# Optimization experiments

Hardware: AMD Instinct MI355X
Metric: run time of the kernel (lower is better)

## Reference

```python
import jax, jax.numpy as jnp
import numpy as np

DK = 64  # embedding_size / h = 1024 / 16


def setup_inputs() -> dict:
    key = jax.random.key(0)
    k1, k2, k3 = jax.random.split(key, 3)
    S = 8192
    return {
        "q": jax.random.normal(k1, (S, DK), dtype=jnp.float32),
        "k": jax.random.normal(k2, (S, DK), dtype=jnp.float32),
        "v": jax.random.normal(k3, (S, DK), dtype=jnp.float32),
    }


def reference(q, k, v):
    # scores: [S, S]; NOTE: source scales by 1/dk (not 1/sqrt(dk)) — kept faithful.
    qk = jnp.matmul(q, k.T) * (1.0 / DK)
    S = qk.shape[0]
    # causal mask: position (i, j) allowed iff i >= j (0 added), else -inf
    i = jnp.arange(S)[:, None]
    j = jnp.arange(S)[None, :]
    qk = jnp.where(i >= j, qk, -jnp.inf)
    attn = jax.nn.softmax(qk, axis=-1)
    return jnp.matmul(attn, v)
```

## Files before the change

### kernel.cpp

```cpp
#include <hip/hip_runtime.h>
#include <hip/hip_bf16.h>

#define S_LEN 8192
#define DKD   64
#define BM    64
#define BN    64
#define PAD   8
#define LDK   (DKD + PAD)

#define CHUNK 512
#define NC    (S_LEN / CHUNK)
#define NWORK 1088

#define WS_NEED ((size_t)2 * S_LEN * DKD * 2 + (size_t)NC * S_LEN * 4 + (size_t)NC * S_LEN * DKD * 2)

typedef __bf16 bf16x8 __attribute__((ext_vector_type(8)));
typedef float  f32x4  __attribute__((ext_vector_type(4)));
typedef unsigned short ushort8v __attribute__((ext_vector_type(8)));
typedef unsigned short ushort4v __attribute__((ext_vector_type(4)));

__device__ __forceinline__ unsigned short f2bf(float f) {
  union { float f; unsigned u; } v; v.f = f;
  unsigned u = v.u;
  return (unsigned short)((u + 0x7fffu + ((u >> 16) & 1u)) >> 16);
}
__device__ __forceinline__ float bf2f(unsigned short s) {
  union { unsigned u; float f; } v; v.u = ((unsigned)s) << 16;
  return v.f;
}
__device__ __forceinline__ unsigned pk2(float a, float b) {
  union { float f; unsigned u; } x, y; x.f = a; y.f = b;
  return ((x.u + 0x8000u) >> 16) | ((y.u + 0x8000u) & 0xffff0000u);
}
__device__ __forceinline__ bf16x8 q_frag8(const float* p, float sc) {
  float4 u = *(const float4*)p;
  float4 w = *(const float4*)(p + 4);
  union { ushort8v s; bf16x8 b; } r;
  r.s[0] = f2bf(u.x * sc); r.s[1] = f2bf(u.y * sc);
  r.s[2] = f2bf(u.z * sc); r.s[3] = f2bf(u.w * sc);
  r.s[4] = f2bf(w.x * sc); r.s[5] = f2bf(w.y * sc);
  r.s[6] = f2bf(w.z * sc); r.s[7] = f2bf(w.w * sc);
  return r.b;
}

__global__ __launch_bounds__(256) void precompute(const float* __restrict__ k,
                                                  const float* __restrict__ v,
                                                  unsigned short* __restrict__ Kb,
                                                  unsigned short* __restrict__ Vtb) {
  __shared__ unsigned short Ls[64][72];
  const int b = blockIdx.x, tid = threadIdx.x;
  if (blockIdx.y == 0) {
    size_t base = (size_t)b * 64 * DKD;
#pragma unroll
    for (int j = 0; j < 4; ++j) {
      int vi = tid + j * 256;
      float4 x = *(const float4*)(k + base + (size_t)vi * 4);
      ushort4v o = { f2bf(x.x), f2bf(x.y), f2bf(x.z), f2bf(x.w) };
      *(ushort4v*)(Kb + base + (size_t)vi * 4) = o;
    }
  } else {
#pragma unroll
    for (int j = 0; j < 4; ++j) {
      int vi = tid + j * 256;
      int row = vi >> 4, c4 = vi & 15;
      float4 x = *(const float4*)(v + ((size_t)(b * 64 + row)) * DKD + c4 * 4);
      Ls[row][c4 * 4 + 0] = f2bf(x.x);
      Ls[row][c4 * 4 + 1] = f2bf(x.y);
      Ls[row][c4 * 4 + 2] = f2bf(x.z);
      Ls[row][c4 * 4 + 3] = f2bf(x.w);
    }
    __syncthreads();
#pragma unroll
    for (int j = 0; j < 4; ++j) {
      int ci = tid + j * 256;
      int d = ci >> 4, c0 = ci & 15;
      int kl = c0 * 4;
      int s0 = ((((kl & 7) >> 2) + 2 * (kl >> 5)) << 4) + (((kl >> 3) & 3) << 2);
      ushort4v o = { Ls[s0][d], Ls[s0 + 1][d], Ls[s0 + 2][d], Ls[s0 + 3][d] };
      *(ushort4v*)(Vtb + (size_t)d * S_LEN + b * 64 + kl) = o;
    }
  }
}

__global__ __launch_bounds__(256) void attn_partial(const float* __restrict__ qg,
                                                    const unsigned short* __restrict__ Kb,
                                                    const unsigned short* __restrict__ Vtb,
                                                    unsigned short* __restrict__ Opart,
                                                    float* __restrict__ l_ws) {
  const int w = blockIdx.x;
  int g = (int)((sqrtf((float)w + 1.0f) - 1.0f) * 0.5f);
  while (4 * (g + 1) * (g + 2) <= w) ++g;
  while (4 * g * (g + 1) > w) --g;
  const int r0  = w - 4 * g * (g + 1);
  const int qq  = r0 / (g + 1);
  const int qt  = 8 * g + qq;
  const int cch = r0 - qq * (g + 1);

  const int q0 = qt * BM, chunk0 = cch * CHUNK;
  const int n_kt = min(CHUNK / BN, qt - 8 * cch + 1);

  __shared__ __align__(16) unsigned short Ks[BN][LDK];
  __shared__ __align__(16) unsigned short Vts[DKD][LDK];

  const int tid = threadIdx.x, wave = tid >> 6, lane = tid & 63;
  const int col = lane & 15, quad = lane >> 4;

  const int qidx = q0 + wave * 16 + col;
  const float* qp = qg + (size_t)qidx * DKD;
  bf16x8 b0 = q_frag8(qp + quad * 8, 1.0f / 64.0f);
  bf16x8 b1 = q_frag8(qp + 32 + quad * 8, 1.0f / 64.0f);

  const int srow0 = tid >> 3, sch = tid & 7;
  const int srow1 = srow0 + 32;
  const unsigned short* kbase = Kb + (size_t)chunk0 * DKD;
  const unsigned short* vbase = Vtb + chunk0;

  {
    *(ushort8v*)&Ks[srow0][sch * 8]  = *(const ushort8v*)(kbase + (size_t)srow0 * DKD + sch * 8);
    *(ushort8v*)&Ks[srow1][sch * 8]  = *(const ushort8v*)(kbase + (size_t)srow1 * DKD + sch * 8);
    *(ushort8v*)&Vts[srow0][sch * 8] = *(const ushort8v*)(vbase + (size_t)srow0 * S_LEN + sch * 8);
    *(ushort8v*)&Vts[srow1][sch * 8] = *(const ushort8v*)(vbase + (size_t)srow1 * S_LEN + sch * 8);
  }
  __syncthreads();

  float lsum = 0.0f;
  f32x4 Of[4];
#pragma unroll
  for (int i = 0; i < 4; ++i) Of[i] = f32x4{0.0f, 0.0f, 0.0f, 0.0f};

  ushort8v Kp0, Kp1, Vp0, Vp1;
  for (int it = 0; it < n_kt; ++it) {
    const int k0 = chunk0 + it * BN;
    const bool pf = (it + 1 < n_kt);

    if (pf) {
      const size_t noff = (size_t)(it + 1) * BN;
      Kp0 = *(const ushort8v*)(kbase + (noff + srow0) * DKD + sch * 8);
      Kp1 = *(const ushort8v*)(kbase + (noff + srow1) * DKD + sch * 8);
      Vp0 = *(const ushort8v*)(vbase + (size_t)srow0 * S_LEN + noff + sch * 8);
      Vp1 = *(const ushort8v*)(vbase + (size_t)srow1 * S_LEN + noff + sch * 8);
    }

    f32x4 Sf[4];
#pragma unroll
    for (int t = 0; t < 4; ++t) {
      const unsigned short* kr = &Ks[t * 16 + col][quad * 8];
      f32x4 acc = f32x4{0.0f, 0.0f, 0.0f, 0.0f};
      acc = __builtin_amdgcn_mfma_f32_16x16x32_bf16(*(const bf16x8*)kr, b0, acc, 0, 0, 0);
      acc = __builtin_amdgcn_mfma_f32_16x16x32_bf16(*(const bf16x8*)(kr + 32), b1, acc, 0, 0, 0);
      Sf[t] = acc;
    }

#pragma unroll
    for (int t = 0; t < 4; ++t) {
      int kb = k0 + t * 16 + quad * 4;
#pragma unroll
      for (int r = 0; r < 4; ++r) {
        float p = __expf(Sf[t][r]);
        p = (kb + r <= qidx) ? p : 0.0f;
        Sf[t][r] = p;
        lsum += p;
      }
    }

    union { unsigned u[4]; bf16x8 b; } pa0, pa1;
    pa0.u[0] = pk2(Sf[0][0], Sf[0][1]); pa0.u[1] = pk2(Sf[0][2], Sf[0][3]);
    pa0.u[2] = pk2(Sf[1][0], Sf[1][1]); pa0.u[3] = pk2(Sf[1][2], Sf[1][3]);
    pa1.u[0] = pk2(Sf[2][0], Sf[2][1]); pa1.u[1] = pk2(Sf[2][2], Sf[2][3]);
    pa1.u[2] = pk2(Sf[3][0], Sf[3][1]); pa1.u[3] = pk2(Sf[3][2], Sf[3][3]);

#pragma unroll
    for (int dt = 0; dt < 4; ++dt) {
      const unsigned short* vr = &Vts[dt * 16 + col][quad * 8];
      Of[dt] = __builtin_amdgcn_mfma_f32_16x16x32_bf16(pa0.b, *(const bf16x8*)vr, Of[dt], 0, 0, 0);
      Of[dt] = __builtin_amdgcn_mfma_f32_16x16x32_bf16(pa1.b, *(const bf16x8*)(vr + 32), Of[dt], 0, 0, 0);
    }

    if (pf) {
      __syncthreads();
      *(ushort8v*)&Ks[srow0][sch * 8]  = Kp0;
      *(ushort8v*)&Ks[srow1][sch * 8]  = Kp1;
      *(ushort8v*)&Vts[srow0][sch * 8] = Vp0;
      *(ushort8v*)&Vts[srow1][sch * 8] = Vp1;
      __syncthreads();
    }
  }

  lsum += __shfl_xor(lsum, 16);
  lsum += __shfl_xor(lsum, 32);
  if (lane < 16)
    l_ws[cch * S_LEN + q0 + wave * 16 + lane] = lsum;

#pragma unroll
  for (int r = 0; r < 4; ++r) {
    int rowg = q0 + wave * 16 + quad * 4 + r;
    uint2 o2;
    o2.x = pk2(Of[0][r], Of[1][r]);
    o2.y = pk2(Of[2][r], Of[3][r]);
    *(uint2*)(Opart + ((size_t)cch * S_LEN + rowg) * DKD + col * 4) = o2;
  }
}

__global__ __launch_bounds__(256) void attn_merge(const unsigned short* __restrict__ Opart,
                                                  const float* __restrict__ l_ws,
                                                  float* __restrict__ out) {
  int idx = blockIdx.x * 256 + threadIdx.x;
  int row = idx >> 3, m = idx & 7;
  int nc = (row >> 9) + 1;

  float acc[8] = {0, 0, 0, 0, 0, 0, 0, 0};
  float L = 0.0f;
  for (int c = 0; c < nc; ++c) {
    L += l_ws[c * S_LEN + row];
    ushort8v o = *(const ushort8v*)(Opart + ((size_t)c * S_LEN + row) * DKD + m * 8);
#pragma unroll
    for (int j = 0; j < 8; ++j) acc[j] += bf2f(o[j]);
  }
  float inv = 1.0f / L;
#pragma unroll
  for (int j0 = 0; j0 < 4; ++j0) {
    float2 w2 = { acc[j0] * inv, acc[j0 + 4] * inv };
    *(float2*)(out + (size_t)row * DKD + 16 * j0 + 2 * m) = w2;
  }
}

__global__ __launch_bounds__(128) void attn_fwd(const float* __restrict__ qg,
                                                const float* __restrict__ kg,
                                                const float* __restrict__ vg,
                                                float* __restrict__ out) {
  __shared__ __align__(16) unsigned short Qs[32][LDK];
  __shared__ __align__(16) unsigned short Ksh[BN][LDK];
  __shared__ __align__(16) unsigned short Vt[DKD][LDK];
  __shared__ __align__(16) unsigned short Ps[2][16][LDK];

  const int tid = threadIdx.x, wave = tid >> 6, lane = tid & 63;
  const int col = lane & 15, quad = lane >> 4;
  const int q0 = blockIdx.x * 32;

#pragma unroll
  for (int r = 0; r < 4; ++r) {
    int vi = tid + r * 128;
    int row = vi >> 4, c4 = vi & 15;
    if (row < 32) {
      float4 val = *(const float4*)(qg + (size_t)(q0 + row) * DKD + c4 * 4);
      Qs[row][c4 * 4 + 0] = f2bf(val.x);
      Qs[row][c4 * 4 + 1] = f2bf(val.y);
      Qs[row][c4 * 4 + 2] = f2bf(val.z);
      Qs[row][c4 * 4 + 3] = f2bf(val.w);
    }
  }

  float m_run[4], l_run[4];
  f32x4 Of[4];
#pragma unroll
  for (int i = 0; i < 4; ++i) {
    m_run[i] = -1e30f; l_run[i] = 0.0f;
    Of[i] = f32x4{0.0f, 0.0f, 0.0f, 0.0f};
  }

  const int n_tiles = (q0 + 31) / BN + 1;
  for (int it = 0; it < n_tiles; ++it) {
    __syncthreads();
    const int k0 = it * BN;
#pragma unroll
    for (int r = 0; r < 8; ++r) {
      int vi = tid + r * 128;
      int row = vi >> 4, c4 = vi & 15;
      float4 kv = *(const float4*)(kg + (size_t)(k0 + row) * DKD + c4 * 4);
      Ksh[row][c4 * 4 + 0] = f2bf(kv.x);
      Ksh[row][c4 * 4 + 1] = f2bf(kv.y);
      Ksh[row][c4 * 4 + 2] = f2bf(kv.z);
      Ksh[row][c4 * 4 + 3] = f2bf(kv.w);
      float4 vv = *(const float4*)(vg + (size_t)(k0 + row) * DKD + c4 * 4);
      Vt[c4 * 4 + 0][row] = f2bf(vv.x);
      Vt[c4 * 4 + 1][row] = f2bf(vv.y);
      Vt[c4 * 4 + 2][row] = f2bf(vv.z);
      Vt[c4 * 4 + 3][row] = f2bf(vv.w);
    }
    __syncthreads();

    f32x4 Sf[4];
    const unsigned short* qrow = &Qs[wave * 16 + col][0];
#pragma unroll
    for (int t = 0; t < 4; ++t) {
      f32x4 acc = f32x4{0.0f, 0.0f, 0.0f, 0.0f};
#pragma unroll
      for (int c = 0; c < 2; ++c) {
        bf16x8 a = *(const bf16x8*)(qrow + c * 32 + quad * 8);
        bf16x8 b = *(const bf16x8*)(&Ksh[t * 16 + col][c * 32 + quad * 8]);
        acc = __builtin_amdgcn_mfma_f32_16x16x32_bf16(a, b, acc, 0, 0, 0);
      }
      Sf[t] = acc;
    }

    const float scale = 1.0f / 64.0f;
    float rmax[4] = {-1e30f, -1e30f, -1e30f, -1e30f};
#pragma unroll
    for (int t = 0; t < 4; ++t) {
      int kidx = k0 + t * 16 + col;
#pragma unroll
      for (int r = 0; r < 4; ++r) {
        int qidx = q0 + wave * 16 + quad * 4 + r;
        float s = Sf[t][r] * scale;
        s = (kidx <= qidx) ? s : -1e30f;
        Sf[t][r] = s;
        rmax[r] = fmaxf(rmax[r], s);
      }
    }
#pragma unroll
    for (int off = 1; off <= 8; off <<= 1)
#pragma unroll
      for (int r = 0; r < 4; ++r)
        rmax[r] = fmaxf(rmax[r], __shfl_xor(rmax[r], off));

    float alpha[4], rsum[4];
#pragma unroll
    for (int r = 0; r < 4; ++r) {
      float mn = fmaxf(m_run[r], rmax[r]);
      alpha[r] = __expf(m_run[r] - mn);
      m_run[r] = mn;
      rsum[r] = 0.0f;
    }
#pragma unroll
    for (int t = 0; t < 4; ++t)
#pragma unroll
      for (int r = 0; r < 4; ++r) {
        float p = __expf(Sf[t][r] - m_run[r]);
        Sf[t][r] = p;
        rsum[r] += p;
      }
#pragma unroll
    for (int off = 1; off <= 8; off <<= 1)
#pragma unroll
      for (int r = 0; r < 4; ++r)
        rsum[r] += __shfl_xor(rsum[r], off);
#pragma unroll
    for (int r = 0; r < 4; ++r)
      l_run[r] = l_run[r] * alpha[r] + rsum[r];
#pragma unroll
    for (int dt = 0; dt < 4; ++dt)
#pragma unroll
      for (int r = 0; r < 4; ++r)
        Of[dt][r] *= alpha[r];

#pragma unroll
    for (int t = 0; t < 4; ++t)
#pragma unroll
      for (int r = 0; r < 4; ++r)
        Ps[wave][quad * 4 + r][t * 16 + col] = f2bf(Sf[t][r]);
    __syncthreads();

    const unsigned short* prow = &Ps[wave][col][0];
#pragma unroll
    for (int dt = 0; dt < 4; ++dt) {
#pragma unroll
      for (int c = 0; c < 2; ++c) {
        bf16x8 a = *(const bf16x8*)(prow + c * 32 + quad * 8);
        bf16x8 b = *(const bf16x8*)(&Vt[dt * 16 + col][c * 32 + quad * 8]);
        Of[dt] = __builtin_amdgcn_mfma_f32_16x16x32_bf16(a, b, Of[dt], 0, 0, 0);
      }
    }
  }

#pragma unroll
  for (int r = 0; r < 4; ++r) {
    float inv = 1.0f / l_run[r];
    int qrow_g = q0 + wave * 16 + quad * 4 + r;
#pragma unroll
    for (int dt = 0; dt < 4; ++dt)
      out[(size_t)qrow_g * DKD + dt * 16 + col] = Of[dt][r] * inv;
  }
}

extern "C" void kernel_launch(void* const* d_in, const int* in_sizes, int n_in,
                              void* d_out, int out_size, void* d_ws, size_t ws_size,
                              hipStream_t stream) {
  const float* q = (const float*)d_in[0];
  const float* k = (const float*)d_in[1];
  const float* v = (const float*)d_in[2];
  float* out = (float*)d_out;

  if (ws_size >= WS_NEED) {
    unsigned short* Kb  = (unsigned short*)d_ws;
    unsigned short* Vtb = Kb + (size_t)S_LEN * DKD;
    float* l_ws         = (float*)(Vtb + (size_t)S_LEN * DKD);
    unsigned short* Opart = (unsigned short*)(l_ws + (size_t)NC * S_LEN);

    hipLaunchKernelGGL(precompute, dim3(S_LEN / 64, 2), dim3(256), 0, stream, k, v, Kb, Vtb);
    hipLaunchKernelGGL(attn_partial, dim3(NWORK), dim3(256), 0, stream,
                       q, Kb, Vtb, Opart, l_ws);
    hipLaunchKernelGGL(attn_merge, dim3(S_LEN * 8 / 256), dim3(256), 0, stream,
                       Opart, l_ws, out);
  } else {
    hipLaunchKernelGGL(attn_fwd, dim3(S_LEN / 32), dim3(128), 0, stream, q, k, v, out);
  }
}
```

Measured before the change: 90.05 us.

## Widen key tile to 128 and schedule heaviest work items first

Doubles the key/value tile per inner iteration from 64 to 128. The V-transpose precompute is reworked so each block handles a 128-key by 32-dim slab with a matching permuted layout. This halves the number of barrier-separated iterations and raises MFMA work per synchronisation, at the cost of more registers and LDS per block. Work items are also issued in reverse order so the longest causal rows start first, which should reduce tail imbalance. Causal masking now operates at 128-key granularity, so slightly more fully-masked keys are computed.

After: 90.57 us. No clear change (+0.6%).

```diff
diff --git a/kernel.cpp b/kernel.cpp
--- a/kernel.cpp
+++ b/kernel.cpp
@@ -4,7 +4,7 @@
 #define S_LEN 8192
 #define DKD   64
 #define BM    64
-#define BN    64
+#define BN    128
 #define PAD   8
 #define LDK   (DKD + PAD)
 
@@ -47,7 +47,7 @@
                                                   const float* __restrict__ v,
                                                   unsigned short* __restrict__ Kb,
                                                   unsigned short* __restrict__ Vtb) {
-  __shared__ unsigned short Ls[64][72];
+  __shared__ unsigned short Ls[128][36];
   const int b = blockIdx.x, tid = threadIdx.x;
   if (blockIdx.y == 0) {
     size_t base = (size_t)b * 64 * DKD;
@@ -59,11 +59,12 @@
       *(ushort4v*)(Kb + base + (size_t)vi * 4) = o;
     }
   } else {
+    const int tile = b >> 1, dh = (b & 1) * 32;
 #pragma unroll
     for (int j = 0; j < 4; ++j) {
       int vi = tid + j * 256;
-      int row = vi >> 4, c4 = vi & 15;
-      float4 x = *(const float4*)(v + ((size_t)(b * 64 + row)) * DKD + c4 * 4);
+      int row = vi >> 3, c4 = vi & 7;
+      float4 x = *(const float4*)(v + ((size_t)(tile * 128 + row)) * DKD + dh + c4 * 4);
       Ls[row][c4 * 4 + 0] = f2bf(x.x);
       Ls[row][c4 * 4 + 1] = f2bf(x.y);
       Ls[row][c4 * 4 + 2] = f2bf(x.z);
@@ -73,11 +74,10 @@
 #pragma unroll
     for (int j = 0; j < 4; ++j) {
       int ci = tid + j * 256;
-      int d = ci >> 4, c0 = ci & 15;
-      int kl = c0 * 4;
-      int s0 = ((((kl & 7) >> 2) + 2 * (kl >> 5)) << 4) + (((kl >> 3) & 3) << 2);
-      ushort4v o = { Ls[s0][d], Ls[s0 + 1][d], Ls[s0 + 2][d], Ls[s0 + 3][d] };
-      *(ushort4v*)(Vtb + (size_t)d * S_LEN + b * 64 + kl) = o;
+      int dloc = ci >> 5, kq = ci & 31;
+      int s0 = 32 * (kq >> 3) + 16 * (kq & 1) + 4 * ((kq >> 1) & 3);
+      ushort4v o = { Ls[s0][dloc], Ls[s0 + 1][dloc], Ls[s0 + 2][dloc], Ls[s0 + 3][dloc] };
+      *(ushort4v*)(Vtb + (size_t)(dh + dloc) * S_LEN + tile * 128 + kq * 4) = o;
     }
   }
 }
@@ -87,20 +87,20 @@
                                                     const unsigned short* __restrict__ Vtb,
                                                     unsigned short* __restrict__ Opart,
                                                     float* __restrict__ l_ws) {
-  const int w = blockIdx.x;
-  int g = (int)((sqrtf((float)w + 1.0f) - 1.0f) * 0.5f);
-  while (4 * (g + 1) * (g + 2) <= w) ++g;
-  while (4 * g * (g + 1) > w) --g;
-  const int r0  = w - 4 * g * (g + 1);
+  const int wr = (NWORK - 1) - blockIdx.x;
+  int g = (int)((sqrtf((float)wr + 1.0f) - 1.0f) * 0.5f);
+  while (4 * (g + 1) * (g + 2) <= wr) ++g;
+  while (4 * g * (g + 1) > wr) --g;
+  const int r0  = wr - 4 * g * (g + 1);
   const int qq  = r0 / (g + 1);
   const int qt  = 8 * g + qq;
   const int cch = r0 - qq * (g + 1);
 
   const int q0 = qt * BM, chunk0 = cch * CHUNK;
-  const int n_kt = min(CHUNK / BN, qt - 8 * cch + 1);
-
-  __shared__ __align__(16) unsigned short Ks[BN][LDK];
-  __shared__ __align__(16) unsigned short Vts[DKD][LDK];
+  const int n_kt = min(CHUNK / BN, ((q0 - chunk0) >> 7) + 1);
+
+  __shared__ __align__(16) unsigned short Ks[BN][72];
+  __shared__ __align__(16) unsigned short Vts[DKD][136];
 
   const int tid = threadIdx.x, wave = tid >> 6, lane = tid & 63;
   const int col = lane & 15, quad = lane >> 4;
@@ -110,16 +110,17 @@
   bf16x8 b0 = q_frag8(qp + quad * 8, 1.0f / 64.0f);
   bf16x8 b1 = q_frag8(qp + 32 + quad * 8, 1.0f / 64.0f);
 
-  const int srow0 = tid >> 3, sch = tid & 7;
-  const int srow1 = srow0 + 32;
+  const int krow = tid >> 3, kch = tid & 7;
+  const int vd   = tid >> 4, vch = tid & 15;
   const unsigned short* kbase = Kb + (size_t)chunk0 * DKD;
   const unsigned short* vbase = Vtb + chunk0;
 
-  {
-    *(ushort8v*)&Ks[srow0][sch * 8]  = *(const ushort8v*)(kbase + (size_t)srow0 * DKD + sch * 8);
-    *(ushort8v*)&Ks[srow1][sch * 8]  = *(const ushort8v*)(kbase + (size_t)srow1 * DKD + sch * 8);
-    *(ushort8v*)&Vts[srow0][sch * 8] = *(const ushort8v*)(vbase + (size_t)srow0 * S_LEN + sch * 8);
-    *(ushort8v*)&Vts[srow1][sch * 8] = *(const ushort8v*)(vbase + (size_t)srow1 * S_LEN + sch * 8);
+#pragma unroll
+  for (int j = 0; j < 4; ++j) {
+    *(ushort8v*)&Ks[krow + j * 32][kch * 8] =
+        *(const ushort8v*)(kbase + (size_t)(krow + j * 32) * DKD + kch * 8);
+    *(ushort8v*)&Vts[vd + j * 16][vch * 8] =
+        *(const ushort8v*)(vbase + (size_t)(vd + j * 16) * S_LEN + vch * 8);
   }
   __syncthreads();
 
@@ -128,22 +129,23 @@
 #pragma unroll
   for (int i = 0; i < 4; ++i) Of[i] = f32x4{0.0f, 0.0f, 0.0f, 0.0f};
 
-  ushort8v Kp0, Kp1, Vp0, Vp1;
+  ushort8v Kp[4], Vp[4];
   for (int it = 0; it < n_kt; ++it) {
     const int k0 = chunk0 + it * BN;
     const bool pf = (it + 1 < n_kt);
 
     if (pf) {
       const size_t noff = (size_t)(it + 1) * BN;
-      Kp0 = *(const ushort8v*)(kbase + (noff + srow0) * DKD + sch * 8);
-      Kp1 = *(const ushort8v*)(kbase + (noff + srow1) * DKD + sch * 8);
-      Vp0 = *(const ushort8v*)(vbase + (size_t)srow0 * S_LEN + noff + sch * 8);
-      Vp1 = *(const ushort8v*)(vbase + (size_t)srow1 * S_LEN + noff + sch * 8);
-    }
-
-    f32x4 Sf[4];
-#pragma unroll
-    for (int t = 0; t < 4; ++t) {
+#pragma unroll
+      for (int j = 0; j < 4; ++j) {
+        Kp[j] = *(const ushort8v*)(kbase + (noff + krow + j * 32) * DKD + kch * 8);
+        Vp[j] = *(const ushort8v*)(vbase + (size_t)(vd + j * 16) * S_LEN + noff + vch * 8);
+      }
+    }
+
+    f32x4 Sf[8];
+#pragma unroll
+    for (int t = 0; t < 8; ++t) {
       const unsigned short* kr = &Ks[t * 16 + col][quad * 8];
       f32x4 acc = f32x4{0.0f, 0.0f, 0.0f, 0.0f};
       acc = __builtin_amdgcn_mfma_f32_16x16x32_bf16(*(const bf16x8*)kr, b0, acc, 0, 0, 0);
@@ -152,7 +154,7 @@
     }
 
 #pragma unroll
-    for (int t = 0; t < 4; ++t) {
+    for (int t = 0; t < 8; ++t) {
       int kb = k0 + t * 16 + quad * 4;
 #pragma unroll
       for (int r = 0; r < 4; ++r) {
@@ -163,25 +165,30 @@
       }
     }
 
-    union { unsigned u[4]; bf16x8 b; } pa0, pa1;
-    pa0.u[0] = pk2(Sf[0][0], Sf[0][1]); pa0.u[1] = pk2(Sf[0][2], Sf[0][3]);
-    pa0.u[2] = pk2(Sf[1][0], Sf[1][1]); pa0.u[3] = pk2(Sf[1][2], Sf[1][3]);
-    pa1.u[0] = pk2(Sf[2][0], Sf[2][1]); pa1.u[1] = pk2(Sf[2][2], Sf[2][3]);
-    pa1.u[2] = pk2(Sf[3][0], Sf[3][1]); pa1.u[3] = pk2(Sf[3][2], Sf[3][3]);
+    union { unsigned u[4]; bf16x8 b; } pa[4];
+#pragma unroll
+    for (int m = 0; m < 4; ++m) {
+      pa[m].u[0] = pk2(Sf[2 * m][0], Sf[2 * m][1]);
+      pa[m].u[1] = pk2(Sf[2 * m][2], Sf[2 * m][3]);
+      pa[m].u[2] = pk2(Sf[2 * m + 1][0], Sf[2 * m + 1][1]);
+      pa[m].u[3] = pk2(Sf[2 * m + 1][2], Sf[2 * m + 1][3]);
+    }
 
 #pragma unroll
     for (int dt = 0; dt < 4; ++dt) {
       const unsigned short* vr = &Vts[dt * 16 + col][quad * 8];
-      Of[dt] = __builtin_amdgcn_mfma_f32_16x16x32_bf16(pa0.b, *(const bf16x8*)vr, Of[dt], 0, 0, 0);
-      Of[dt] = __builtin_amdgcn_mfma_f32_16x16x32_bf16(pa1.b, *(const bf16x8*)(vr + 32), Of[dt], 0, 0, 0);
+#pragma unroll
+      for (int m = 0; m < 4; ++m)
+        Of[dt] = __builtin_amdgcn_mfma_f32_16x16x32_bf16(pa[m].b, *(const bf16x8*)(vr + m * 32), Of[dt], 0, 0, 0);
     }
 
     if (pf) {
       __syncthreads();
-      *(ushort8v*)&Ks[srow0][sch * 8]  = Kp0;
-      *(ushort8v*)&Ks[srow1][sch * 8]  = Kp1;
-      *(ushort8v*)&Vts[srow0][sch * 8] = Vp0;
-      *(ushort8v*)&Vts[srow1][sch * 8] = Vp1;
+#pragma unroll
+      for (int j = 0; j < 4; ++j) {
+        *(ushort8v*)&Ks[krow + j * 32][kch * 8]  = Kp[j];
+        *(ushort8v*)&Vts[vd + j * 16][vch * 8]   = Vp[j];
+      }
       __syncthreads();
     }
   }
@@ -229,7 +236,7 @@
                                                 const float* __restrict__ vg,
                                                 float* __restrict__ out) {
   __shared__ __align__(16) unsigned short Qs[32][LDK];
-  __shared__ __align__(16) unsigned short Ksh[BN][LDK];
+  __shared__ __align__(16) unsigned short Ksh[64][LDK];
   __shared__ __align__(16) unsigned short Vt[DKD][LDK];
   __shared__ __align__(16) unsigned short Ps[2][16][LDK];
 
@@ -258,10 +265,10 @@
     Of[i] = f32x4{0.0f, 0.0f, 0.0f, 0.0f};
   }
 
-  const int n_tiles = (q0 + 31) / BN + 1;
+  const int n_tiles = (q0 + 31) / 64 + 1;
   for (int it = 0; it < n_tiles; ++it) {
     __syncthreads();
-    const int k0 = it * BN;
+    const int k0 = it * 64;
 #pragma unroll
     for (int r = 0; r < 8; ++r) {
       int vi = tid + r * 128;
@@ -386,7 +393,7 @@
     float* l_ws         = (float*)(Vtb + (size_t)S_LEN * DKD);
     unsigned short* Opart = (unsigned short*)(l_ws + (size_t)NC * S_LEN);
 
-    hipLaunchKernelGGL(precompute, dim3(S_LEN / 64, 2), dim3(256), 0, stream, k, v, Kb, Vtb);
+    hipLaunchKernelGGL(precompute, dim3(128, 2), dim3(256), 0, stream, k, v, Kb, Vtb);
     hipLaunchKernelGGL(attn_partial, dim3(NWORK), dim3(256), 0, stream,
                        q, Kb, Vtb, Opart, l_ws);
     hipLaunchKernelGGL(attn_merge, dim3(S_LEN * 8 / 256), dim3(256), 0, stream,
```
